# Performance work log

Measured on AMD Instinct MI355X. Metric: run time of the kernel, lower is better.

Reference implementation:

```python
import jax, jax.numpy as jnp
import numpy as np

EMBED_DIM = 2048
NUM_HEADS = 16
NUM_KV_HEADS = 4
KEY_DIM = EMBED_DIM // NUM_HEADS  # 128
B, S = 2, 2048


def setup_inputs() -> dict:
    key = jax.random.key(0)
    ks = jax.random.split(key, 8)
    kv_dim = KEY_DIM * NUM_KV_HEADS
    sc_in = 1.0 / np.sqrt(EMBED_DIM)
    return {
        "query": jax.random.normal(ks[0], (B, S, EMBED_DIM), jnp.float32),
        "key": jax.random.normal(ks[1], (B, S, EMBED_DIM), jnp.float32),
        "value": jax.random.normal(ks[2], (B, S, EMBED_DIM), jnp.float32),
        "mask": jnp.ones((B, S), jnp.float32),
        "Wq": jax.random.normal(ks[3], (EMBED_DIM, EMBED_DIM), jnp.float32) * sc_in,
        "Wk": jax.random.normal(ks[4], (EMBED_DIM, kv_dim), jnp.float32) * sc_in,
        "Wv": jax.random.normal(ks[5], (EMBED_DIM, kv_dim), jnp.float32) * sc_in,
        "Wo": jax.random.normal(ks[6], (EMBED_DIM, EMBED_DIM), jnp.float32) * sc_in,
    }


def reference(query, key, value, mask, Wq, Wk, Wv, Wo):
    b, sq, _ = query.shape
    skv = key.shape[1]
    scale = 1.0 / float(KEY_DIM) ** 0.5
    # projections (no bias)
    q = (query @ Wq).reshape(b, sq, NUM_HEADS, KEY_DIM).transpose(0, 2, 1, 3)      # [B,H,Sq,D]
    k = (key @ Wk).reshape(b, skv, NUM_KV_HEADS, KEY_DIM).transpose(0, 2, 1, 3)    # [B,Hkv,Skv,D]
    v = (value @ Wv).reshape(b, skv, NUM_KV_HEADS, KEY_DIM).transpose(0, 2, 1, 3)  # [B,Hkv,Skv,D]
    n_rep = NUM_HEADS // NUM_KV_HEADS
    k_rep = jnp.repeat(k, n_rep, axis=1)  # [B,H,Skv,D]
    v_rep = jnp.repeat(v, n_rep, axis=1)  # [B,H,Skv,D]
    scores = jnp.einsum("bhqd,bhkd->bhqk", q, k_rep) * scale  # [B,H,Sq,Skv]
    scores = scores + (1.0 - mask[:, None, None, :].astype(scores.dtype)) * -1e9
    attn = jax.nn.softmax(scores, axis=-1)
    out = jnp.einsum("bhqk,bhkd->bhqd", attn, v_rep)  # [B,H,Sq,D]
    out = out.transpose(0, 2, 1, 3).reshape(b, sq, EMBED_DIM)
    return out @ Wo
```

## Files before the change

kernel.cpp:

```cpp
#include <hip/hip_runtime.h>
#include <hip/hip_bf16.h>

#define B_    2
#define S_    2048
#define E_    2048
#define H_    16
#define HKV_  4
#define D_    128
#define NTOK  4096
#define KVDIM 512

typedef __bf16 bf16x8 __attribute__((ext_vector_type(8)));
typedef __bf16 bf16x4 __attribute__((ext_vector_type(4)));
typedef float  f32x4  __attribute__((ext_vector_type(4)));

__device__ __forceinline__ void async_copy16(const void* g, void* l) {
  __builtin_amdgcn_global_load_lds(
      (const __attribute__((address_space(1))) unsigned int*)g,
      (__attribute__((address_space(3))) unsigned int*)l, 16, 0, 0);
}

__global__ __launch_bounds__(256) void transpose_all(
    const float* __restrict__ Wq, const float* __restrict__ Wk,
    const float* __restrict__ Wv, const float* __restrict__ Wo,
    __bf16* __restrict__ WTq, __bf16* __restrict__ WTk,
    __bf16* __restrict__ WTv, __bf16* __restrict__ WoT) {
  const float* in;
  __bf16* out;
  int C;
  switch (blockIdx.z) {
    case 0:  in = Wq; out = WTq; C = E_;   break;
    case 1:  in = Wk; out = WTk; C = KVDIM; break;
    case 2:  in = Wv; out = WTv; C = KVDIM; break;
    default: in = Wo; out = WoT; C = E_;   break;
  }
  const int c0 = blockIdx.x * 32;
  if (c0 >= C) return;
  const int r0 = blockIdx.y * 32;
  __shared__ float t[32][33];
  const int tr = threadIdx.x >> 3;
  const int tc = (threadIdx.x & 7) * 4;
  const float* ip = in + (size_t)(r0 + tr) * C + c0 + tc;
#pragma unroll
  for (int i = 0; i < 4; ++i) t[tr][tc + i] = ip[i];
  __syncthreads();
  __bf16* op = out + (size_t)(c0 + tr) * E_ + r0 + tc;
#pragma unroll
  for (int i = 0; i < 4; ++i) op[i] = (__bf16)t[tc + i][tr];
}

__global__ __launch_bounds__(256) void convert_q(const float* __restrict__ in,
                                                 __bf16* __restrict__ ob) {
  const size_t i = ((size_t)blockIdx.x * 256 + threadIdx.x) * 8;
  const f32x4 a0 = *(const f32x4*)(in + i);
  const f32x4 a1 = *(const f32x4*)(in + i + 4);
  bf16x8 v;
#pragma unroll
  for (int j = 0; j < 4; ++j) { v[j] = (__bf16)a0[j]; v[4 + j] = (__bf16)a1[j]; }
  *(bf16x8*)(ob + i) = v;
}

__global__ __launch_bounds__(512, 1) void gemm_pipe(
    const __bf16* __restrict__ A, const __bf16* __restrict__ Bt,
    float* __restrict__ Cf, __bf16* __restrict__ Cb, int M, int N, int K,
    int epi) {
  __shared__ __align__(16) __bf16 lds[2 * 24576];

  const int n0 = blockIdx.x * 256;
  const int m0 = blockIdx.y * 128;
  const int tid = threadIdx.x;
  const int w = tid >> 6;
  const int lane = tid & 63;
  const int quad = lane >> 4;
  const int l16 = lane & 15;
  const int wm = w >> 2;
  const int wn = w & 3;
  const int lr = lane >> 3;
  const int ls = lane & 7;

  const __bf16* pa[2];
  const __bf16* pb[4];
#pragma unroll
  for (int r = 0; r < 2; ++r) {
    const int row = r * 64 + w * 8 + lr;
    pa[r] = A + (size_t)(m0 + row) * K + ((ls ^ (row & 7)) * 8);
  }
#pragma unroll
  for (int r = 0; r < 4; ++r) {
    const int row = r * 64 + w * 8 + lr;
    pb[r] = Bt + (size_t)(n0 + row) * K + ((ls ^ (row & 7)) * 8);
  }

  auto stage = [&](int bufi) {
    __bf16* base = lds + bufi * 24576;
#pragma unroll
    for (int r = 0; r < 2; ++r) {
      async_copy16(pa[r], base + (size_t)(r * 64 + w * 8) * 64);
      pa[r] += 64;
    }
#pragma unroll
    for (int r = 0; r < 4; ++r) {
      async_copy16(pb[r], base + 8192 + (size_t)(r * 64 + w * 8) * 64);
      pb[r] += 64;
    }
  };

  f32x4 acc[4][4] = {};
  const int NT = K >> 6;
  const int xr = l16 & 7;

  stage(0);
  stage(1);

  for (int t = 0; t < NT; ++t) {
    if (t < NT - 1) {
      asm volatile("s_waitcnt vmcnt(6)\n\ts_barrier" ::: "memory");
    } else {
      asm volatile("s_waitcnt vmcnt(0)\n\ts_barrier" ::: "memory");
    }
    const __bf16* lA = lds + (t & 1) * 24576;
    const __bf16* lB = lA + 8192;

    bf16x8 af[4][2], bfr[4][2];
#pragma unroll
    for (int f = 0; f < 4; ++f) {
      const int rowb = (wm * 64 + f * 16 + l16) * 64;
#pragma unroll
      for (int ks = 0; ks < 2; ++ks)
        af[f][ks] = *(const bf16x8*)&lA[rowb + (((ks * 4 + quad) ^ xr) * 8)];
    }
#pragma unroll
    for (int g = 0; g < 4; ++g) {
      const int rowb = (wn * 64 + g * 16 + l16) * 64;
#pragma unroll
      for (int ks = 0; ks < 2; ++ks)
        bfr[g][ks] = *(const bf16x8*)&lB[rowb + (((ks * 4 + quad) ^ xr) * 8)];
    }
    asm volatile("s_waitcnt lgkmcnt(0)\n\ts_barrier" ::: "memory");
    if (t + 2 < NT) stage(t & 1);

    __builtin_amdgcn_s_setprio(1);
#pragma unroll
    for (int f = 0; f < 4; ++f)
#pragma unroll
      for (int g = 0; g < 4; ++g) {
        acc[f][g] = __builtin_amdgcn_mfma_f32_16x16x32_bf16(af[f][0], bfr[g][0],
                                                            acc[f][g], 0, 0, 0);
        acc[f][g] = __builtin_amdgcn_mfma_f32_16x16x32_bf16(af[f][1], bfr[g][1],
                                                            acc[f][g], 0, 0, 0);
      }
    __builtin_amdgcn_s_setprio(0);
  }

#pragma unroll
  for (int f = 0; f < 4; ++f) {
#pragma unroll
    for (int g = 0; g < 4; ++g) {
#pragma unroll
      for (int r = 0; r < 4; ++r) {
        const int m = m0 + wm * 64 + f * 16 + quad * 4 + r;
        const int n = n0 + wn * 64 + g * 16 + l16;
        if (epi == 0) Cf[(size_t)m * N + n] = acc[f][g][r];
        else          Cb[(size_t)m * N + n] = (__bf16)acc[f][g][r];
      }
    }
  }
}

__global__ __launch_bounds__(256, 2) void gemm_kv(
    const float* __restrict__ key, const float* __restrict__ value,
    const __bf16* __restrict__ WTk, const __bf16* __restrict__ WTv,
    __bf16* __restrict__ Kp, __bf16* __restrict__ Vt) {
  __shared__ __align__(16) __bf16 As[128 * 32];
  __shared__ __align__(16) __bf16 Bs[128 * 32];

  const int bx = blockIdx.x;
  const float* A;
  const __bf16* Bt;
  int n0, epi;
  if (bx < 4) { A = key;   Bt = WTk; n0 = bx * 128;       epi = 0; }
  else        { A = value; Bt = WTv; n0 = (bx - 4) * 128; epi = 1; }
  const int m0 = blockIdx.y * 128;
  const int K = E_;
  const int N = KVDIM;

  const int tid = threadIdx.x;
  const int w = tid >> 6;
  const int lane = tid & 63;
  const int quad = lane >> 4;
  const int l16 = lane & 15;
  const int wr = w >> 1, wc = w & 1;
  const int brow = lane >> 2;
  const int bcol = (lane & 3) * 8;
  const int arow = lane >> 2;
  const int acol = (lane & 3) * 8;

  f32x4 acc[4][4] = {};

  for (int k0 = 0; k0 < K; k0 += 32) {
    __syncthreads();
#pragma unroll
    for (int c = 0; c < 2; ++c) {
      const int chunk = w * 2 + c;
      const int row = chunk * 16 + brow;
      async_copy16(Bt + (size_t)(n0 + row) * K + k0 + bcol, &Bs[chunk * 512]);
    }
#pragma unroll
    for (int s = 0; s < 2; ++s) {
      const int row = w * 32 + s * 16 + arow;
      const float* src = A + (size_t)(m0 + row) * K + k0 + acol;
      const f32x4 a0 = *(const f32x4*)src;
      const f32x4 a1 = *(const f32x4*)(src + 4);
      bf16x8 v;
#pragma unroll
      for (int j = 0; j < 4; ++j) { v[j] = (__bf16)a0[j]; v[4 + j] = (__bf16)a1[j]; }
      *(bf16x8*)&As[row * 32 + acol] = v;
    }
    __syncthreads();
    bf16x8 af[4], bfr[4];
#pragma unroll
    for (int i = 0; i < 4; ++i)
      af[i] = *(const bf16x8*)&As[(wr * 64 + i * 16 + l16) * 32 + quad * 8];
#pragma unroll
    for (int j = 0; j < 4; ++j)
      bfr[j] = *(const bf16x8*)&Bs[(wc * 64 + j * 16 + l16) * 32 + quad * 8];
#pragma unroll
    for (int i = 0; i < 4; ++i)
#pragma unroll
      for (int j = 0; j < 4; ++j)
        acc[i][j] = __builtin_amdgcn_mfma_f32_16x16x32_bf16(af[i], bfr[j],
                                                            acc[i][j], 0, 0, 0);
  }

#pragma unroll
  for (int i = 0; i < 4; ++i) {
#pragma unroll
    for (int j = 0; j < 4; ++j) {
#pragma unroll
      for (int r = 0; r < 4; ++r) {
        const int m = m0 + wr * 64 + i * 16 + quad * 4 + r;
        const int n = n0 + wc * 64 + j * 16 + l16;
        if (epi == 0) {
          Kp[(size_t)m * N + n] = (__bf16)acc[i][j][r];
        } else {
          const int b = m >> 11, s = m & (S_ - 1);
          Vt[((size_t)((b * HKV_ + (n >> 7)) * D_ + (n & (D_ - 1)))) * S_ + s] =
              (__bf16)acc[i][j][r];
        }
      }
    }
  }
}

__global__ __launch_bounds__(256, 2) void attn_kernel(
    const __bf16* __restrict__ Q, const __bf16* __restrict__ Kp,
    const __bf16* __restrict__ Vt, const float* __restrict__ mask,
    __bf16* __restrict__ Oa) {
  __shared__ __align__(16) __bf16 K_lds[64][136];
  __shared__ __align__(16) __bf16 V_lds[128][72];
  __shared__ __align__(16) __bf16 P_lds[4][32][72];

  const int tid = threadIdx.x;
  const int w = tid >> 6, lane = tid & 63, quad = lane >> 4, l16 = lane & 15;
  const int bh = blockIdx.y;
  const int b = bh >> 4, h = bh & 15, hkv = h >> 2;
  const int q0 = blockIdx.x * 128 + w * 32;

  const __bf16* qbase = Q + (size_t)(b * S_ + q0) * E_ + h * D_;
  bf16x8 qf[2][4];
#pragma unroll
  for (int m = 0; m < 2; ++m)
#pragma unroll
    for (int ks = 0; ks < 4; ++ks)
      qf[m][ks] = *(const bf16x8*)(qbase + (size_t)(m * 16 + l16) * E_ +
                                   ks * 32 + quad * 8);

  const __bf16* kbase = Kp + (size_t)(b * S_) * KVDIM + hkv * D_;
  const __bf16* vbase = Vt + (size_t)((b * HKV_ + hkv) * D_) * S_;
  const float* mbase = mask + b * S_;

  f32x4 o[2][8] = {};
  f32x4 lsum[2] = {};
  const float scale = 0.08838834764831845f;

  for (int kt = 0; kt < S_; kt += 64) {
    __syncthreads();
#pragma unroll
    for (int i = 0; i < 4; ++i) {
      const int r = w * 16 + i * 4 + (lane >> 4);
      bf16x8 kv = *(const bf16x8*)(kbase + (size_t)(kt + r) * KVDIM +
                                   (lane & 15) * 8);
      *(bf16x8*)&K_lds[r][(lane & 15) * 8] = kv;
    }
#pragma unroll
    for (int i = 0; i < 4; ++i) {
      const int r = w * 32 + i * 8 + (lane >> 3);
      bf16x8 vv = *(const bf16x8*)(vbase + (size_t)r * S_ + kt +
                                   (lane & 7) * 8);
      *(bf16x8*)&V_lds[r][(lane & 7) * 8] = vv;
    }
    __syncthreads();

    f32x4 s[2][4] = {};
    __builtin_amdgcn_s_setprio(1);
#pragma unroll
    for (int ks = 0; ks < 4; ++ks) {
#pragma unroll
      for (int n = 0; n < 4; ++n) {
        bf16x8 kf = *(const bf16x8*)&K_lds[n * 16 + l16][ks * 32 + quad * 8];
        s[0][n] = __builtin_amdgcn_mfma_f32_16x16x32_bf16(qf[0][ks], kf,
                                                          s[0][n], 0, 0, 0);
        s[1][n] = __builtin_amdgcn_mfma_f32_16x16x32_bf16(qf[1][ks], kf,
                                                          s[1][n], 0, 0, 0);
      }
    }
    __builtin_amdgcn_s_setprio(0);

    float bias[4];
#pragma unroll
    for (int n = 0; n < 4; ++n)
      bias[n] = (1.0f - mbase[kt + n * 16 + l16]) * -1e9f;
#pragma unroll
    for (int m = 0; m < 2; ++m) {
#pragma unroll
      for (int n = 0; n < 4; ++n) {
#pragma unroll
        for (int r = 0; r < 4; ++r) {
          const float p = __expf(s[m][n][r] * scale + bias[n]);
          lsum[m][r] += p;
          P_lds[w][m * 16 + quad * 4 + r][n * 16 + l16] = (__bf16)p;
        }
      }
    }

    __builtin_amdgcn_s_setprio(1);
#pragma unroll
    for (int ks2 = 0; ks2 < 2; ++ks2) {
      bf16x8 pa[2];
#pragma unroll
      for (int m = 0; m < 2; ++m)
        pa[m] = *(const bf16x8*)&P_lds[w][m * 16 + l16][ks2 * 32 + quad * 8];
#pragma unroll
      for (int dt = 0; dt < 8; ++dt) {
        bf16x8 vf = *(const bf16x8*)&V_lds[dt * 16 + l16][ks2 * 32 + quad * 8];
        o[0][dt] = __builtin_amdgcn_mfma_f32_16x16x32_bf16(pa[0], vf,
                                                           o[0][dt], 0, 0, 0);
        o[1][dt] = __builtin_amdgcn_mfma_f32_16x16x32_bf16(pa[1], vf,
                                                           o[1][dt], 0, 0, 0);
      }
    }
    __builtin_amdgcn_s_setprio(0);
  }

  __bf16* obase = Oa + (size_t)(b * S_ + q0) * E_ + h * D_;
#pragma unroll
  for (int m = 0; m < 2; ++m) {
#pragma unroll
    for (int r = 0; r < 4; ++r) {
      float v = lsum[m][r];
#pragma unroll
      for (int off = 1; off < 16; off <<= 1) v += __shfl_xor(v, off);
      const float inv = 1.0f / v;
#pragma unroll
      for (int dt = 0; dt < 8; ++dt)
        obase[(size_t)(m * 16 + quad * 4 + r) * E_ + dt * 16 + l16] =
            (__bf16)(o[m][dt][r] * inv);
    }
  }
}

extern "C" void kernel_launch(void* const* d_in, const int* in_sizes, int n_in,
                              void* d_out, int out_size, void* d_ws,
                              size_t ws_size, hipStream_t stream) {
  const float* query = (const float*)d_in[0];
  const float* key   = (const float*)d_in[1];
  const float* value = (const float*)d_in[2];
  const float* mask  = (const float*)d_in[3];
  const float* Wq    = (const float*)d_in[4];
  const float* Wk    = (const float*)d_in[5];
  const float* Wv    = (const float*)d_in[6];
  const float* Wo    = (const float*)d_in[7];
  float* out = (float*)d_out;

  __bf16* ws   = (__bf16*)d_ws;
  __bf16* Qp   = ws;
  __bf16* Kp   = Qp + (size_t)NTOK * E_;
  __bf16* Vt   = Kp + (size_t)NTOK * KVDIM;
  __bf16* WoT  = Vt + (size_t)NTOK * KVDIM;
  __bf16* WTq  = WoT + (size_t)E_ * E_;
  __bf16* WTk  = WTq + (size_t)E_ * E_;
  __bf16* WTv  = WTk + (size_t)KVDIM * E_;
  __bf16* Attn = WTq;
  __bf16* qb   = (__bf16*)d_out;

  transpose_all<<<dim3(64, 64, 4), 256, 0, stream>>>(Wq, Wk, Wv, Wo,
                                                     WTq, WTk, WTv, WoT);
  convert_q<<<dim3(4096), 256, 0, stream>>>(query, qb);
  gemm_kv<<<dim3(8, 32), 256, 0, stream>>>(key, value, WTk, WTv, Kp, Vt);
  gemm_pipe<<<dim3(E_ / 256, NTOK / 128), 512, 0, stream>>>(
      qb, WTq, nullptr, Qp, NTOK, E_, E_, 1);
  attn_kernel<<<dim3(S_ / 128, B_ * H_), 256, 0, stream>>>(Qp, Kp, Vt, mask,
                                                           Attn);
  gemm_pipe<<<dim3(E_ / 256, NTOK / 128), 512, 0, stream>>>(
      Attn, WoT, out, nullptr, NTOK, E_, E_, 0);
}
```

Measured before the change: 409.2 us.

## Split GEMM k-loop into two half-phases with staggered A/B async loads

Restructures the bf16 GEMM main loop so each iteration processes the A fragments in two halves, issuing the next A tile load and the next-next B tile load at different points between the MFMA blocks. The aim is to overlap global-to-LDS copies and LDS fragment reads with MFMA work, in the style of a ping-pong schedule, and to cut register pressure from holding all A fragments at once. It adds more barriers per iteration and depends on fragile vmcnt accounting, which risks races or stalls if the counts are wrong.

Result: no change. 411.2 us (+0.5%).

```diff
diff --git a/kernel.cpp b/kernel.cpp
--- a/kernel.cpp
+++ b/kernel.cpp
@@ -91,16 +91,19 @@
     pb[r] = Bt + (size_t)(n0 + row) * K + ((ls ^ (row & 7)) * 8);
   }
 
-  auto stage = [&](int bufi) {
+  auto stageA = [&](int bufi) {
     __bf16* base = lds + bufi * 24576;
 #pragma unroll
     for (int r = 0; r < 2; ++r) {
       async_copy16(pa[r], base + (size_t)(r * 64 + w * 8) * 64);
       pa[r] += 64;
     }
+  };
+  auto stageB = [&](int bufi) {
+    __bf16* base = lds + bufi * 24576 + 8192;
 #pragma unroll
     for (int r = 0; r < 4; ++r) {
-      async_copy16(pb[r], base + 8192 + (size_t)(r * 64 + w * 8) * 64);
+      async_copy16(pb[r], base + (size_t)(r * 64 + w * 8) * 64);
       pb[r] += 64;
     }
   };
@@ -109,21 +112,19 @@
   const int NT = K >> 6;
   const int xr = l16 & 7;
 
-  stage(0);
-  stage(1);
+  stageA(0);
+  stageB(0);
+  stageB(1);
+  asm volatile("s_waitcnt vmcnt(4)" ::: "memory");
+  __builtin_amdgcn_s_barrier();
 
   for (int t = 0; t < NT; ++t) {
-    if (t < NT - 1) {
-      asm volatile("s_waitcnt vmcnt(6)\n\ts_barrier" ::: "memory");
-    } else {
-      asm volatile("s_waitcnt vmcnt(0)\n\ts_barrier" ::: "memory");
-    }
     const __bf16* lA = lds + (t & 1) * 24576;
     const __bf16* lB = lA + 8192;
 
-    bf16x8 af[4][2], bfr[4][2];
-#pragma unroll
-    for (int f = 0; f < 4; ++f) {
+    bf16x8 af[2][2], bfr[4][2];
+#pragma unroll
+    for (int f = 0; f < 2; ++f) {
       const int rowb = (wm * 64 + f * 16 + l16) * 64;
 #pragma unroll
       for (int ks = 0; ks < 2; ++ks)
@@ -136,12 +137,13 @@
       for (int ks = 0; ks < 2; ++ks)
         bfr[g][ks] = *(const bf16x8*)&lB[rowb + (((ks * 4 + quad) ^ xr) * 8)];
     }
-    asm volatile("s_waitcnt lgkmcnt(0)\n\ts_barrier" ::: "memory");
-    if (t + 2 < NT) stage(t & 1);
-
+    if (t + 1 < NT) stageA((t + 1) & 1);
+    __builtin_amdgcn_s_barrier();
+    asm volatile("s_waitcnt lgkmcnt(0)" ::: "memory");
+    __builtin_amdgcn_sched_barrier(0);
     __builtin_amdgcn_s_setprio(1);
 #pragma unroll
-    for (int f = 0; f < 4; ++f)
+    for (int f = 0; f < 2; ++f)
 #pragma unroll
       for (int g = 0; g < 4; ++g) {
         acc[f][g] = __builtin_amdgcn_mfma_f32_16x16x32_bf16(af[f][0], bfr[g][0],
@@ -150,6 +152,39 @@
                                                             acc[f][g], 0, 0, 0);
       }
     __builtin_amdgcn_s_setprio(0);
+    __builtin_amdgcn_s_barrier();
+
+    bf16x8 ah[2][2];
+#pragma unroll
+    for (int f = 0; f < 2; ++f) {
+      const int rowb = (wm * 64 + (f + 2) * 16 + l16) * 64;
+#pragma unroll
+      for (int ks = 0; ks < 2; ++ks)
+        ah[f][ks] = *(const bf16x8*)&lA[rowb + (((ks * 4 + quad) ^ xr) * 8)];
+    }
+    if (t + 2 < NT) stageB(t & 1);
+    __builtin_amdgcn_s_barrier();
+    asm volatile("s_waitcnt lgkmcnt(0)" ::: "memory");
+    __builtin_amdgcn_sched_barrier(0);
+    __builtin_amdgcn_s_setprio(1);
+#pragma unroll
+    for (int f = 0; f < 2; ++f)
+#pragma unroll
+      for (int g = 0; g < 4; ++g) {
+        acc[f + 2][g] = __builtin_amdgcn_mfma_f32_16x16x32_bf16(
+            ah[f][0], bfr[g][0], acc[f + 2][g], 0, 0, 0);
+        acc[f + 2][g] = __builtin_amdgcn_mfma_f32_16x16x32_bf16(
+            ah[f][1], bfr[g][1], acc[f + 2][g], 0, 0, 0);
+      }
+    __builtin_amdgcn_s_setprio(0);
+
+    if (t + 2 < NT) {
+      asm volatile("s_waitcnt vmcnt(4)" ::: "memory");
+      __builtin_amdgcn_s_barrier();
+    } else if (t + 1 < NT) {
+      asm volatile("s_waitcnt vmcnt(0)" ::: "memory");
+      __builtin_amdgcn_s_barrier();
+    }
   }
 
 #pragma unroll
```
